# Performance work log

Hardware: AMD Instinct MI355X
Metric: run time of the kernel (lower is better)

## Reference

```python
import jax, jax.numpy as jnp
import numpy as np
from jax import lax

BN_EPS = 1e-3
SLOPE = 0.1
CLUSTER_TEMP = 30.0
K = 16
FEAT = 4096  # 8*8*64


def conv_bn_lrelu(x, w, b, g, beta, m, v):
    # Conv2d stride 2, padding 1 (NCHW / OIHW), then eval-mode BatchNorm, then LeakyReLU.
    y = lax.conv_general_dilated(x, w, window_strides=(2, 2), padding=((1, 1), (1, 1)),
                                 dimension_numbers=("NCHW", "OIHW", "NCHW"))
    y = y + b[None, :, None, None]
    scale = g / jnp.sqrt(v + BN_EPS)
    y = y * scale[None, :, None, None] + (beta - m * scale)[None, :, None, None]
    return jnp.where(y > 0, y, SLOPE * y)


def soft_kmeans(data, mu, num_iter, ct):
    # Row L2-normalize (equivalent to diag(1/||x||) @ data)
    data = data / jnp.linalg.norm(data, axis=1, keepdims=True)
    for _ in range(num_iter):
        dist = data @ mu.T                      # [N, K]
        r = jax.nn.softmax(ct * dist, axis=1)   # [N, K]
        mu = (r.T @ data) / r.sum(axis=0)[:, None]  # [K, F]
    dist = data @ mu.T
    r = jax.nn.softmax(ct * dist, axis=1)
    return mu, r, dist


def setup_inputs() -> dict:
    key = jax.random.key(0)
    ks = jax.random.split(key, 12)
    d = {}
    d["x"] = jax.random.normal(ks[0], (256, 3, 64, 64), dtype=jnp.float32)
    # conv1: 3 -> 128
    d["conv1_w"] = jax.random.normal(ks[1], (128, 3, 3, 3), dtype=jnp.float32) * 0.05
    d["conv1_b"] = jnp.zeros((128,), jnp.float32)
    d["bn1_g"] = jnp.ones((128,), jnp.float32)
    d["bn1_b"] = jnp.zeros((128,), jnp.float32)
    d["bn1_m"] = jax.random.normal(ks[2], (128,), dtype=jnp.float32) * 0.1
    d["bn1_v"] = jax.random.uniform(ks[3], (128,), minval=0.5, maxval=1.5, dtype=jnp.float32)
    # conv2: 128 -> 256
    d["conv2_w"] = jax.random.normal(ks[4], (256, 128, 3, 3), dtype=jnp.float32) * 0.02
    d["conv2_b"] = jnp.zeros((256,), jnp.float32)
    d["bn2_g"] = jnp.ones((256,), jnp.float32)
    d["bn2_b"] = jnp.zeros((256,), jnp.float32)
    d["bn2_m"] = jax.random.normal(ks[5], (256,), dtype=jnp.float32) * 0.1
    d["bn2_v"] = jax.random.uniform(ks[6], (256,), minval=0.5, maxval=1.5, dtype=jnp.float32)
    # conv3: 256 -> 64
    d["conv3_w"] = jax.random.normal(ks[7], (64, 256, 3, 3), dtype=jnp.float32) * 0.02
    d["conv3_b"] = jnp.zeros((64,), jnp.float32)
    d["bn3_g"] = jnp.ones((64,), jnp.float32)
    d["bn3_b"] = jnp.zeros((64,), jnp.float32)
    d["bn3_m"] = jax.random.normal(ks[8], (64,), dtype=jnp.float32) * 0.1
    d["bn3_v"] = jax.random.uniform(ks[9], (64,), minval=0.5, maxval=1.5, dtype=jnp.float32)
    # initial cluster centers, torch.rand(K, F)
    d["mu0"] = jax.random.uniform(ks[10], (K, FEAT), dtype=jnp.float32)
    d["num_iter"] = 10
    return d


def reference(x, conv1_w, conv1_b, bn1_g, bn1_b, bn1_m, bn1_v,
              conv2_w, conv2_b, bn2_g, bn2_b, bn2_m, bn2_v,
              conv3_w, conv3_b, bn3_g, bn3_b, bn3_m, bn3_v,
              mu0, num_iter):
    h = conv_bn_lrelu(x, conv1_w, conv1_b, bn1_g, bn1_b, bn1_m, bn1_v)   # [B,128,32,32]
    h = conv_bn_lrelu(h, conv2_w, conv2_b, bn2_g, bn2_b, bn2_m, bn2_v)   # [B,256,16,16]
    h = conv_bn_lrelu(h, conv3_w, conv3_b, bn3_g, bn3_b, bn3_m, bn3_v)   # [B,64,8,8]
    embeds = h.reshape(-1, FEAT)                                          # [B, 4096]
    mu_init, _, _ = soft_kmeans(embeds, mu0, num_iter, CLUSTER_TEMP)
    _, r, _ = soft_kmeans(embeds, lax.stop_gradient(mu_init), 1, CLUSTER_TEMP)
    return r
```

## Files before the change

kernel.cpp:

```cpp
#include <hip/hip_runtime.h>
#include <stdint.h>
#include <stddef.h>

typedef unsigned short u16;
typedef __attribute__((ext_vector_type(8))) short short8;
typedef __attribute__((ext_vector_type(4))) float f32x4;
typedef __attribute__((ext_vector_type(4))) int int4v;

__device__ __forceinline__ float bf2f(u16 u) {
    unsigned x = ((unsigned)u) << 16;
    return __uint_as_float(x);
}
__device__ __forceinline__ u16 f2bf(float f) {
    unsigned x = __float_as_uint(f);
    unsigned r = (x + 0x7fffu + ((x >> 16) & 1u)) >> 16;
    return (u16)r;
}
__device__ __forceinline__ float ldin(const void* p, size_t i, int isbf) {
    return isbf ? bf2f(((const u16*)p)[i]) : ((const float*)p)[i];
}
__device__ __forceinline__ int detect_bf(const void* v1) {
    const u16* ub = (const u16*)v1;
    int ok = 1;
#pragma unroll
    for (int i = 0; i < 16; i++) {
        float f = bf2f(ub[i]);
        if (!(f >= 0.4f && f <= 1.6f)) ok = 0;
    }
    return ok;
}
__device__ __forceinline__ int sw(int r, int c8) {
    return r * 32 + (((c8) ^ (r & 3)) << 3);
}

struct PrepArgs {
    const void *w1, *w2, *w3;
    u16 *W1p, *W2p, *W3p;
    const void *b1, *g1, *be1, *m1, *v1;
    const void *b2, *g2, *be2, *m2, *v2;
    const void *b3, *g3, *be3, *m3, *v3;
    float *es1, *esh1, *es2, *esh2, *es3, *esh3;
    u16 *zb;
};
__device__ __forceinline__ void packw_body(const void* src, u16* dst, int CI, int Kp,
                                           int total, int blk, int t, int isbf) {
    int p = blk * 256 + t;
    if (p >= total) return;
    int co = p / Kp, k = p - co * Kp;
    int tap = k / CI, ci = k - tap * CI;
    u16 v = 0;
    if (tap < 9) {
        size_t si = (size_t)(co * CI + ci) * 9 + tap;
        v = isbf ? ((const u16*)src)[si] : f2bf(((const float*)src)[si]);
    }
    dst[p] = v;
}
__global__ __launch_bounds__(256) void kprep_all(PrepArgs A) {
    int b = blockIdx.x, t = threadIdx.x;
    int isbf = detect_bf(A.v1);
    if (b < 1152) {
        packw_body(A.w2, A.W2p, 128, 1152, 256 * 1152, b, t, isbf);
    } else if (b < 1728) {
        packw_body(A.w3, A.W3p, 256, 2304, 64 * 2304, b - 1152, t, isbf);
    } else if (b < 1744) {
        packw_body(A.w1, A.W1p, 3, 32, 128 * 32, b - 1728, t, isbf);
    } else {
        if (b == 1745) A.zb[t] = 0;
        int u = (b - 1744) * 256 + t;
        const void *bb, *g, *be, *m, *v;
        float *es, *esh;
        int c;
        if (u < 128)      { c = u;       bb=A.b1; g=A.g1; be=A.be1; m=A.m1; v=A.v1; es=A.es1; esh=A.esh1; }
        else if (u < 384) { c = u - 128; bb=A.b2; g=A.g2; be=A.be2; m=A.m2; v=A.v2; es=A.es2; esh=A.esh2; }
        else if (u < 448) { c = u - 384; bb=A.b3; g=A.g3; be=A.be3; m=A.m3; v=A.v3; es=A.es3; esh=A.esh3; }
        else return;
        float sc = ldin(g, c, isbf) / sqrtf(ldin(v, c, isbf) + 1e-3f);
        float sh = (ldin(bb, c, isbf) - ldin(m, c, isbf)) * sc + ldin(be, c, isbf);
        es[c] = sc;
        esh[c] = sh;
    }
}

__global__ void kfallback(u16* __restrict__ out) {
    int i = blockIdx.x * 256 + threadIdx.x;
    if (i < 4096) out[i] = f2bf(0.0625f);
}

__global__ __launch_bounds__(256) void im2col1(const void* __restrict__ x,
                                               u16* __restrict__ A1,
                                               const void* __restrict__ v1ref) {
    int n = blockIdx.x, t = threadIdx.x;
    int isbf = detect_bf(v1ref);
    __shared__ u16 xs[3 * 64 * 64];
    if (isbf) {
        const u16* xp = (const u16*)x + (size_t)n * 12288;
#pragma unroll
        for (int i = t * 8; i < 12288; i += 2048)
            *(int4v*)&xs[i] = *(const int4v*)&xp[i];
    } else {
        const float* xp = (const float*)x + (size_t)n * 12288;
#pragma unroll
        for (int i = t * 4; i < 12288; i += 1024) {
            float4 v = *(const float4*)&xp[i];
            xs[i] = f2bf(v.x); xs[i + 1] = f2bf(v.y);
            xs[i + 2] = f2bf(v.z); xs[i + 3] = f2bf(v.w);
        }
    }
    __syncthreads();
#pragma unroll
    for (int rr = 0; rr < 4; rr++) {
        int m = rr * 256 + t;
        int ox = m & 31, oy = m >> 5;
        alignas(16) u16 row[32];
#pragma unroll
        for (int k = 0; k < 32; k++) {
            u16 val = 0;
            if (k < 27) {
                int tap = k / 3, ci = k - 3 * tap;
                int ky = tap / 3, kx = tap - 3 * ky;
                int iy = 2 * oy - 1 + ky, ix = 2 * ox - 1 + kx;
                if ((unsigned)iy < 64u && (unsigned)ix < 64u)
                    val = xs[ci * 4096 + iy * 64 + ix];
            }
            row[k] = val;
        }
        int4v* dst = (int4v*)(A1 + ((size_t)n * 1024 + m) * 32);
        const int4v* srcv = (const int4v*)row;
#pragma unroll
        for (int q = 0; q < 4; q++) dst[q] = srcv[q];
    }
}

__global__ __launch_bounds__(256) void gemm_conv1(
    const u16* __restrict__ A1, const u16* __restrict__ W,
    const float* __restrict__ es, const float* __restrict__ esh,
    u16* __restrict__ OutB) {
    alignas(16) __shared__ u16 As[128 * 32];
    alignas(16) __shared__ u16 Bs[128 * 32];
    const int t = threadIdx.x;
    const int m0 = blockIdx.x * 128;
    const int lane = t & 63, w = t >> 6;
    const int wm = w & 1, wn = w >> 1;
    const int rA = t >> 2, c8 = t & 3, koff = c8 * 8;

#pragma unroll
    for (int j = 0; j < 2; j++) {
        int4v va = *(const int4v*)(A1 + (size_t)(m0 + j * 64 + rA) * 32 + koff);
        *(int4v*)&As[sw(j * 64 + rA, c8)] = va;
        int4v vb = *(const int4v*)(W + (size_t)(j * 64 + rA) * 32 + koff);
        *(int4v*)&Bs[sw(j * 64 + rA, c8)] = vb;
    }
    __syncthreads();
    const int qc = lane >> 4, fr = lane & 15;
    short8 af[4], bf[4];
#pragma unroll
    for (int i = 0; i < 4; i++) af[i] = *(const short8*)&As[sw(wm * 64 + i * 16 + fr, qc)];
#pragma unroll
    for (int j = 0; j < 4; j++) bf[j] = *(const short8*)&Bs[sw(wn * 64 + j * 16 + fr, qc)];
    f32x4 acc[4][4];
#pragma unroll
    for (int i = 0; i < 4; i++)
#pragma unroll
        for (int j = 0; j < 4; j++) {
#pragma unroll
            for (int q = 0; q < 4; q++) acc[i][j][q] = 0.f;
            acc[i][j] = __builtin_amdgcn_mfma_f32_16x16x32_bf16(af[i], bf[j], acc[i][j], 0, 0, 0);
        }
    float scv[4], shv[4];
#pragma unroll
    for (int j = 0; j < 4; j++) {
        int c = wn * 64 + j * 16 + fr;
        scv[j] = es[c];
        shv[j] = esh[c];
    }
#pragma unroll
    for (int i = 0; i < 4; i++) {
#pragma unroll
        for (int rg = 0; rg < 4; rg++) {
            int m = m0 + wm * 64 + i * 16 + qc * 4 + rg;
            int ox = m & 31, oy = (m >> 5) & 31, n = m >> 10;
            u16* orow = OutB + ((size_t)(n * 32 + oy) * 32 + ox) * 128 + wn * 64 + fr;
#pragma unroll
            for (int j = 0; j < 4; j++) {
                float v = acc[i][j][rg] * scv[j] + shv[j];
                v = (v > 0.f) ? v : 0.1f * v;
                orow[j * 16] = f2bf(v);
            }
        }
    }
}

__global__ __launch_bounds__(512, 2) void gemm_conv2(
    const u16* __restrict__ h1, const u16* __restrict__ W,
    const float* __restrict__ es, const float* __restrict__ esh,
    u16* __restrict__ OutB, const u16* __restrict__ zb) {
    alignas(16) __shared__ u16 smem[4 * 16384];
    u16* const Ab0 = smem;
    u16* const Ab1 = smem + 16384;
    u16* const Bb0 = smem + 32768;
    u16* const Bb1 = smem + 49152;

    const int t = threadIdx.x;
    const int w = t >> 6, l = t & 63;
    const int img = blockIdx.x;
    const int wm = w >> 2, wn = w & 3;
    const int fr = l & 15, qc = l >> 4;

    int aiy0[4], aix0[4], ac8e[4];
    int brow[4];
#pragma unroll
    for (int i = 0; i < 4; ++i) {
        int gi = w * 256 + i * 64 + l;
        int r = gi >> 3, c8d = gi & 7;
        int c8s = c8d ^ (r & 7);
        int oy = r >> 4, ox = r & 15;
        aiy0[i] = 2 * oy - 1;
        aix0[i] = 2 * ox - 1;
        ac8e[i] = c8s * 8;
        brow[i] = r * 1152 + c8s * 8;
    }
    auto mkA = [&](int i, int ky, int kx) -> const u16* {
        int iy = aiy0[i] + ky, ix = aix0[i] + kx;
        if ((unsigned)iy < 32u && (unsigned)ix < 32u)
            return h1 + (size_t)(((img * 32 + iy) * 32 + ix) * 128 + ac8e[i]);
        return zb;
    };
    auto stage = [&](const u16* src, u16* ldsbase, int i) {
        __builtin_amdgcn_global_load_lds(
            (const __attribute__((address_space(1))) void*)src,
            (__attribute__((address_space(3))) void*)(ldsbase + (w * 4 + i) * 512),
            16, 0, 0);
    };

    f32x4 acc[8][4];
#pragma unroll
    for (int mi = 0; mi < 8; ++mi)
#pragma unroll
        for (int nj = 0; nj < 4; ++nj)
#pragma unroll
            for (int q = 0; q < 4; ++q) acc[mi][nj][q] = 0.0f;

    auto do_tile = [&](const u16* A, const u16* B) {
#pragma unroll
        for (int kk = 0; kk < 2; ++kk) {
            const int c8 = kk * 4 + qc;
            short8 a[8], b[4];
#pragma unroll
            for (int q = 0; q < 8; ++q) {
                int row = wm * 128 + q * 16 + fr;
                a[q] = *(const short8*)(A + row * 64 + ((c8 ^ (row & 7)) << 3));
            }
#pragma unroll
            for (int j = 0; j < 4; ++j) {
                int row = wn * 64 + j * 16 + fr;
                b[j] = *(const short8*)(B + row * 64 + ((c8 ^ (row & 7)) << 3));
            }
            __builtin_amdgcn_s_setprio(1);
#pragma unroll
            for (int q = 0; q < 8; ++q)
#pragma unroll
                for (int j = 0; j < 4; ++j)
                    acc[q][j] = __builtin_amdgcn_mfma_f32_16x16x32_bf16(
                        a[q], b[j], acc[q][j], 0, 0, 0);
            __builtin_amdgcn_s_setprio(0);
        }
    };

    const u16* pcur[4];
#pragma unroll
    for (int i = 0; i < 4; ++i) pcur[i] = mkA(i, 0, 0);
#pragma unroll
    for (int i = 0; i < 4; ++i) {
        stage(pcur[i], Ab0, i);
        stage(W + brow[i], Bb0, i);
    }

    for (int tap = 0; tap < 9; ++tap) {
        __syncthreads();
#pragma unroll
        for (int i = 0; i < 4; ++i) {
            stage(pcur[i] + 64, Ab1, i);
            stage(W + brow[i] + (2 * tap + 1) * 64, Bb1, i);
        }
        do_tile(Ab0, Bb0);
        __syncthreads();
        if (tap < 8) {
            const int tap2 = tap + 1;
            const int ky2 = (tap2 >= 6) ? 2 : (tap2 >= 3) ? 1 : 0;
            const int kx2 = tap2 - 3 * ky2;
#pragma unroll
            for (int i = 0; i < 4; ++i) pcur[i] = mkA(i, ky2, kx2);
#pragma unroll
            for (int i = 0; i < 4; ++i) {
                stage(pcur[i], Ab0, i);
                stage(W + brow[i] + (2 * tap + 2) * 64, Bb0, i);
            }
        }
        do_tile(Ab1, Bb1);
    }

    float scv[4], shv[4];
#pragma unroll
    for (int nj = 0; nj < 4; ++nj) {
        int c = wn * 64 + nj * 16 + fr;
        scv[nj] = es[c];
        shv[nj] = esh[c];
    }
#pragma unroll
    for (int mi = 0; mi < 8; ++mi) {
#pragma unroll
        for (int rg = 0; rg < 4; ++rg) {
            int r = wm * 128 + mi * 16 + qc * 4 + rg;
            u16* orow = OutB + ((size_t)img * 256 + r) * 256 + wn * 64 + fr;
#pragma unroll
            for (int nj = 0; nj < 4; ++nj) {
                float v = acc[mi][nj][rg] * scv[nj] + shv[nj];
                v = (v > 0.f) ? v : 0.1f * v;
                orow[nj * 16] = f2bf(v);
            }
        }
    }
}

__global__ __launch_bounds__(256) void gemm_conv3f(
    const u16* __restrict__ Asrc, const u16* __restrict__ W,
    const float* __restrict__ es3, const float* __restrict__ esh3,
    float* __restrict__ dat, u16* __restrict__ datbf) {
    constexpr int CIN = 256, KTOT = 2304, IH = 16;
    constexpr int CC = 8, SM = 2, SN = 2;

    alignas(16) __shared__ u16 As[64 * 32];
    alignas(16) __shared__ u16 Bs[64 * 32];
    __shared__ float red[4];

    const int t = threadIdx.x;
    const int lid = blockIdx.x;
    const int xcd = lid & 7, slot = lid >> 3;
    const int img = xcd * 32 + slot;
    const int m0 = img * 64;
    const int lane = t & 63, w = t >> 6;
    const int wm = w & 1, wn = w >> 1;
    const int rA = t >> 2, c8 = t & 3, koff = c8 * 8;
    const int fr = lane & 15, qc = lane >> 4;

    f32x4 acc[SM][SN];
#pragma unroll
    for (int i = 0; i < SM; i++)
#pragma unroll
        for (int j = 0; j < SN; j++)
#pragma unroll
            for (int q = 0; q < 4; q++) acc[i][j][q] = 0.0f;

    const int aox = rA & 7, aoy = (rA >> 3) & 7;
    auto mkoffs = [&](int tap) -> int {
        int ky = tap / 3, kx = tap - 3 * ky;
        int iy = 2 * aoy - 1 + ky, ix = 2 * aox - 1 + kx;
        if ((unsigned)iy < (unsigned)IH && (unsigned)ix < (unsigned)IH)
            return ((img * IH + iy) * IH + ix) * CIN;
        return -0x40000000;
    };
    const u16* Wrow = W + (size_t)rA * KTOT + koff;

    int offs_cur = mkoffs(0), offs_nxt;
    const int4v zerov = (int4v){0, 0, 0, 0};
    int4v bufA[2], bufB[2];
#pragma unroll
    for (int pp = 0; pp < 2; pp++) {
        bufA[pp] = (offs_cur >= 0)
                       ? *(const int4v*)(Asrc + offs_cur + pp * 32 + koff)
                       : zerov;
        bufB[pp] = *(const int4v*)(Wrow + pp * 32);
    }

    int flat = 0;
    for (int tap = 0; tap < 9; tap++) {
        offs_nxt = (tap < 8) ? mkoffs(tap + 1) : -0x40000000;
#pragma unroll
        for (int cc = 0; cc < CC; cc++, flat++) {
            const int pb_ = flat & 1;
            *(int4v*)&As[sw(rA, c8)] = bufA[pb_];
            *(int4v*)&Bs[sw(rA, c8)] = bufB[pb_];
            __syncthreads();
            {
                const int cc2 = cc + 2;
                const bool intap = (cc2 < CC);
                const int cci = intap ? cc2 : cc2 - CC;
                int o = intap ? offs_cur : offs_nxt;
                bufA[pb_] = (o >= 0) ? *(const int4v*)(Asrc + o + cci * 32 + koff) : zerov;
                const bool wvalid = intap || (tap < 8);
                const int wk = (intap ? tap : tap + 1) * CIN + cci * 32;
                bufB[pb_] = wvalid ? *(const int4v*)(Wrow + wk) : zerov;
            }
            short8 af[SM], bf[SN];
#pragma unroll
            for (int i = 0; i < SM; i++)
                af[i] = *(const short8*)&As[sw(wm * 32 + i * 16 + fr, qc)];
#pragma unroll
            for (int j = 0; j < SN; j++)
                bf[j] = *(const short8*)&Bs[sw(wn * 32 + j * 16 + fr, qc)];
#pragma unroll
            for (int i = 0; i < SM; i++)
#pragma unroll
                for (int j = 0; j < SN; j++)
                    acc[i][j] = __builtin_amdgcn_mfma_f32_16x16x32_bf16(
                        af[i], bf[j], acc[i][j], 0, 0, 0);
            __syncthreads();
        }
        offs_cur = offs_nxt;
    }

    float vals[SM][SN][4];
    float ssq = 0.f;
#pragma unroll
    for (int j = 0; j < SN; j++) {
        int c = wn * 32 + j * 16 + fr;
        float sc = es3[c], sh = esh3[c];
#pragma unroll
        for (int i = 0; i < SM; i++) {
#pragma unroll
            for (int rg = 0; rg < 4; rg++) {
                float v = acc[i][j][rg] * sc + sh;
                v = (v > 0.f) ? v : 0.1f * v;
                vals[i][j][rg] = v;
                ssq += v * v;
            }
        }
    }
#pragma unroll
    for (int off = 32; off > 0; off >>= 1) ssq += __shfl_xor(ssq, off);
    if (lane == 0) red[w] = ssq;
    __syncthreads();
    float inv = 1.0f / sqrtf(red[0] + red[1] + red[2] + red[3]);
#pragma unroll
    for (int j = 0; j < SN; j++) {
        int c = wn * 32 + j * 16 + fr;
#pragma unroll
        for (int i = 0; i < SM; i++) {
#pragma unroll
            for (int rg = 0; rg < 4; rg++) {
                int row = wm * 32 + i * 16 + qc * 4 + rg;
                size_t idx = (size_t)img * 4096 + c * 64 + row;
                float v = vals[i][j][rg] * inv;
                dat[idx] = v;
                datbf[idx] = f2bf(v);
            }
        }
    }
}

__global__ __launch_bounds__(256) void kgr(const u16* __restrict__ dbf,
                                           const float* __restrict__ dat,
                                           const void* __restrict__ mu0,
                                           u16* __restrict__ Ghi,
                                           u16* __restrict__ Glo,
                                           float* __restrict__ rb0,
                                           const void* __restrict__ v1ref) {
    const int b = blockIdx.x, t = threadIdx.x;
    alignas(16) __shared__ u16 As[64 * 32];
    alignas(16) __shared__ u16 Bs[64 * 32];
    __shared__ float part[16][4];
    __shared__ float ds[16];

    if (b < 16) {
        const int m0 = (b & 3) * 64, n0 = (b >> 2) * 64;
        const int lane = t & 63, w = t >> 6;
        const int wm = w & 1, wn = w >> 1;
        const int rA = t >> 2, c8 = t & 3, koff = c8 * 8;

        f32x4 acc[2][2];
#pragma unroll
        for (int i = 0; i < 2; i++)
#pragma unroll
            for (int j = 0; j < 2; j++)
#pragma unroll
                for (int q = 0; q < 4; q++) acc[i][j][q] = 0.0f;

        int4v pa = *(const int4v*)(dbf + (size_t)(m0 + rA) * 4096 + koff);
        int4v pb = *(const int4v*)(dbf + (size_t)(n0 + rA) * 4096 + koff);
        for (int it = 0; it < 128; it++) {
            *(int4v*)&As[sw(rA, c8)] = pa;
            *(int4v*)&Bs[sw(rA, c8)] = pb;
            __syncthreads();
            if (it + 1 < 128) {
                int k = (it + 1) * 32 + koff;
                pa = *(const int4v*)(dbf + (size_t)(m0 + rA) * 4096 + k);
                pb = *(const int4v*)(dbf + (size_t)(n0 + rA) * 4096 + k);
            }
            const int qc = lane >> 4, fr = lane & 15;
            short8 af[2], bf[2];
#pragma unroll
            for (int i = 0; i < 2; i++) af[i] = *(const short8*)&As[sw(wm * 32 + i * 16 + fr, qc)];
#pragma unroll
            for (int j = 0; j < 2; j++) bf[j] = *(const short8*)&Bs[sw(wn * 32 + j * 16 + fr, qc)];
#pragma unroll
            for (int i = 0; i < 2; i++)
#pragma unroll
                for (int j = 0; j < 2; j++)
                    acc[i][j] = __builtin_amdgcn_mfma_f32_16x16x32_bf16(af[i], bf[j], acc[i][j], 0, 0, 0);
            if (it + 1 < 128) __syncthreads();
        }
#pragma unroll
        for (int j = 0; j < 2; j++) {
            int c = n0 + wn * 32 + j * 16 + (lane & 15);
#pragma unroll
            for (int i = 0; i < 2; i++)
#pragma unroll
                for (int rg = 0; rg < 4; rg++) {
                    int row = m0 + wm * 32 + i * 16 + (lane >> 4) * 4 + rg;
                    float v = acc[i][j][rg];
                    u16 hi = f2bf(v);
                    u16 lo = f2bf(v - bf2f(hi));
                    Ghi[(size_t)row * 256 + c] = hi;
                    Glo[(size_t)row * 256 + c] = lo;
                }
        }
    } else {
        const int n = b - 16;
        const int isbf = detect_bf(v1ref);
        const int lane = t & 63, wv = t >> 6;
        float d[16];
#pragma unroll
        for (int j = 0; j < 16; j++) d[j] = dat[(size_t)n * 4096 + j * 256 + t];
#pragma unroll
        for (int k = 0; k < 16; k++) {
            float a = 0.f;
            if (isbf) {
                const u16* mp = (const u16*)mu0 + (size_t)k * 4096;
#pragma unroll
                for (int j = 0; j < 16; j++) a = fmaf(d[j], bf2f(mp[j * 256 + t]), a);
            } else {
                const float* mp = (const float*)mu0 + (size_t)k * 4096;
#pragma unroll
                for (int j = 0; j < 16; j++) a = fmaf(d[j], mp[j * 256 + t], a);
            }
#pragma unroll
            for (int off = 32; off > 0; off >>= 1) a += __shfl_xor(a, off);
            if (lane == 0) part[k][wv] = a;
        }
        __syncthreads();
        if (t < 16) {
            float dk = part[t][0] + part[t][1] + part[t][2] + part[t][3];
            ds[t] = dk;
            __syncthreads();
            float mx = -1e30f;
#pragma unroll
            for (int j = 0; j < 16; j++) mx = fmaxf(mx, ds[j]);
            float sum = 0.f;
#pragma unroll
            for (int j = 0; j < 16; j++) sum += __expf(30.f * (ds[j] - mx));
            rb0[n * 16 + t] = __expf(30.f * (dk - mx)) / sum;
        }
    }
}

__global__ __launch_bounds__(1024) void kmiter(const u16* __restrict__ Ghi,
                                               const u16* __restrict__ Glo,
                                               const float* __restrict__ rb0,
                                               void* __restrict__ dout,
                                               const void* __restrict__ v1ref) {
    const int t = threadIdx.x;
    const int isbf = detect_bf(v1ref);
    const int lane = t & 63, w = t >> 6;
    const int i0 = w * 16;
    const int col = lane & 15;
    const int q = lane >> 4;

    __shared__ float rf[4096];
    __shared__ u16 rThi[16 * 264];
    __shared__ u16 rTlo[16 * 264];
    __shared__ float part[16][17];
    __shared__ float rs[16];

    for (int idx = t; idx < 4096; idx += 1024) {
        float v = rb0[idx];
        rf[idx] = v;
        u16 hi = f2bf(v);
        rThi[(idx & 15) * 264 + (idx >> 4)] = hi;
        rTlo[(idx & 15) * 264 + (idx >> 4)] = f2bf(v - bf2f(hi));
    }
    __syncthreads();

    const u16* Ahirow = Ghi + (size_t)(i0 + col) * 256 + q * 8;
    const u16* Alorow = Glo + (size_t)(i0 + col) * 256 + q * 8;
    for (int iter = 0; iter < 11; iter++) {
        f32x4 acc = {0.f, 0.f, 0.f, 0.f};
#pragma unroll
        for (int ks = 0; ks < 256; ks += 32) {
            short8 ah = *(const short8*)(Ahirow + ks);
            short8 al = *(const short8*)(Alorow + ks);
            short8 bh = *(const short8*)&rThi[col * 264 + ks + q * 8];
            short8 bl = *(const short8*)&rTlo[col * 264 + ks + q * 8];
            acc = __builtin_amdgcn_mfma_f32_16x16x32_bf16(ah, bh, acc, 0, 0, 0);
            acc = __builtin_amdgcn_mfma_f32_16x16x32_bf16(al, bh, acc, 0, 0, 0);
            acc = __builtin_amdgcn_mfma_f32_16x16x32_bf16(ah, bl, acc, 0, 0, 0);
        }
        if (t < 256) {
            int kk = t & 15, g = t >> 4;
            float psum = 0.f;
#pragma unroll
            for (int nn = 0; nn < 16; nn++) psum += rf[(g * 16 + nn) * 16 + kk];
            part[kk][g] = psum;
        }
        __syncthreads();
        if (t < 16) {
            float ssum = 0.f;
#pragma unroll
            for (int g = 0; g < 16; g++) ssum += part[t][g];
            rs[t] = ssum;
        }
        __syncthreads();
        float rsc = rs[col];
        float rv[4];
#pragma unroll
        for (int rg = 0; rg < 4; rg++) {
            float dk = acc[rg] / rsc;
            float mx = dk;
#pragma unroll
            for (int o = 1; o < 16; o <<= 1) mx = fmaxf(mx, __shfl_xor(mx, o));
            float e = __expf(30.f * (dk - mx));
            float ssum = e;
#pragma unroll
            for (int o = 1; o < 16; o <<= 1) ssum += __shfl_xor(ssum, o);
            rv[rg] = e / ssum;
        }
        if (iter < 10) {
            __syncthreads();
#pragma unroll
            for (int rg = 0; rg < 4; rg++) {
                int row = i0 + q * 4 + rg;
                float v = rv[rg];
                rf[row * 16 + col] = v;
                u16 hi = f2bf(v);
                rThi[col * 264 + row] = hi;
                rTlo[col * 264 + row] = f2bf(v - bf2f(hi));
            }
            __syncthreads();
        } else {
#pragma unroll
            for (int rg = 0; rg < 4; rg++) {
                int row = i0 + q * 4 + rg;
                if (isbf) ((u16*)dout)[row * 16 + col] = f2bf(rv[rg]);
                else ((float*)dout)[row * 16 + col] = rv[rg];
            }
        }
    }
}

extern "C" void kernel_launch(void* const* d_in, const int* in_sizes, int n_in,
                              void* d_out, int out_size, void* d_ws, size_t ws_size,
                              hipStream_t stream) {
    const void* x   = d_in[0];
    const void* w1  = d_in[1];
    const void* b1  = d_in[2];
    const void* g1  = d_in[3];
    const void* be1 = d_in[4];
    const void* m1  = d_in[5];
    const void* v1  = d_in[6];
    const void* w2  = d_in[7];
    const void* b2  = d_in[8];
    const void* g2  = d_in[9];
    const void* be2 = d_in[10];
    const void* m2  = d_in[11];
    const void* v2  = d_in[12];
    const void* w3  = d_in[13];
    const void* b3  = d_in[14];
    const void* g3  = d_in[15];
    const void* be3 = d_in[16];
    const void* m3  = d_in[17];
    const void* v3  = d_in[18];
    const void* mu0 = d_in[19];

    char* p = (char*)d_ws;
    size_t used = 0;
    auto alloc = [&](size_t bytes) -> char* {
        char* q = p;
        size_t rb = (bytes + 255) & ~(size_t)255;
        p += rb;
        used += rb;
        return q;
    };
    float* rb0 = (float*)alloc(4096 * 4);
    u16* Ghi = (u16*)alloc((size_t)65536 * 2);
    u16* Glo = (u16*)alloc((size_t)65536 * 2);
    u16* W1p = (u16*)alloc((size_t)128 * 32 * 2);
    u16* W2p = (u16*)alloc((size_t)256 * 1152 * 2);
    u16* W3p = (u16*)alloc((size_t)64 * 2304 * 2);
    float* es1 = (float*)alloc(128 * 4);
    float* esh1 = (float*)alloc(128 * 4);
    float* es2 = (float*)alloc(256 * 4);
    float* esh2 = (float*)alloc(256 * 4);
    float* es3 = (float*)alloc(64 * 4);
    float* esh3 = (float*)alloc(64 * 4);
    u16* zb = (u16*)alloc(512);
    const size_t R1 = (size_t)256 * 32 * 32 * 128 * 2;
    const size_t R2 = (size_t)256 * 16 * 16 * 256 * 2;
    char* reg1 = alloc(R1);
    char* reg2 = alloc(R2);
    u16* h1 = (u16*)reg1;
    u16* A1 = (u16*)reg2;
    u16* h2 = (u16*)reg2;
    float* dat = (float*)reg1;
    u16* datbf = (u16*)(reg1 + 4194304);

    if (used > ws_size) {
        kfallback<<<16, 256, 0, stream>>>((u16*)d_out);
        return;
    }

    PrepArgs pa = {w1, w2, w3, W1p, W2p, W3p,
                   b1, g1, be1, m1, v1, b2, g2, be2, m2, v2, b3, g3, be3, m3, v3,
                   es1, esh1, es2, esh2, es3, esh3, zb};
    kprep_all<<<1746, 256, 0, stream>>>(pa);
    im2col1<<<256, 256, 0, stream>>>(x, A1, v1);
    gemm_conv1<<<dim3(2048), 256, 0, stream>>>(A1, W1p, es1, esh1, h1);
    gemm_conv2<<<dim3(256), 512, 0, stream>>>(h1, W2p, es2, esh2, h2, zb);
    gemm_conv3f<<<dim3(256), 256, 0, stream>>>(h2, W3p, es3, esh3, dat, datbf);
    kgr<<<dim3(272), 256, 0, stream>>>(datbf, dat, mu0, Ghi, Glo, rb0, v1);
    kmiter<<<1, 1024, 0, stream>>>(Ghi, Glo, rb0, d_out, v1);
}
```

Baseline: 277.6 us.

## Drop LDS staging in Gram GEMM and hoist G fragments into registers in kmiter

The Gram-matrix blocks of kgr now load MFMA fragments straight from global memory instead of staging tiles through shared memory with two barriers per k-step. kmiter keeps its Ghi/Glo fragments in registers across all 11 iterations rather than reloading them from global each time. It also computes the column sums of r with shuffles and a per-wave partial array, which removes the extra barriers and the rf buffer. The costs are more register pressure and global loads that are no longer shared or coalesced through LDS.

```diff
diff --git a/kernel.cpp b/kernel.cpp
--- a/kernel.cpp
+++ b/kernel.cpp
@@ -456,8 +456,6 @@
                                            float* __restrict__ rb0,
                                            const void* __restrict__ v1ref) {
     const int b = blockIdx.x, t = threadIdx.x;
-    alignas(16) __shared__ u16 As[64 * 32];
-    alignas(16) __shared__ u16 Bs[64 * 32];
     __shared__ float part[16][4];
     __shared__ float ds[16];
 
@@ -465,7 +463,7 @@
         const int m0 = (b & 3) * 64, n0 = (b >> 2) * 64;
         const int lane = t & 63, w = t >> 6;
         const int wm = w & 1, wn = w >> 1;
-        const int rA = t >> 2, c8 = t & 3, koff = c8 * 8;
+        const int fr = lane & 15, qc = lane >> 4;
 
         f32x4 acc[2][2];
 #pragma unroll
@@ -475,38 +473,32 @@
 #pragma unroll
                 for (int q = 0; q < 4; q++) acc[i][j][q] = 0.0f;
 
-        int4v pa = *(const int4v*)(dbf + (size_t)(m0 + rA) * 4096 + koff);
-        int4v pb = *(const int4v*)(dbf + (size_t)(n0 + rA) * 4096 + koff);
-        for (int it = 0; it < 128; it++) {
-            *(int4v*)&As[sw(rA, c8)] = pa;
-            *(int4v*)&Bs[sw(rA, c8)] = pb;
-            __syncthreads();
-            if (it + 1 < 128) {
-                int k = (it + 1) * 32 + koff;
-                pa = *(const int4v*)(dbf + (size_t)(m0 + rA) * 4096 + k);
-                pb = *(const int4v*)(dbf + (size_t)(n0 + rA) * 4096 + k);
-            }
-            const int qc = lane >> 4, fr = lane & 15;
-            short8 af[2], bf[2];
-#pragma unroll
-            for (int i = 0; i < 2; i++) af[i] = *(const short8*)&As[sw(wm * 32 + i * 16 + fr, qc)];
-#pragma unroll
-            for (int j = 0; j < 2; j++) bf[j] = *(const short8*)&Bs[sw(wn * 32 + j * 16 + fr, qc)];
+        const u16* a0p = dbf + (size_t)(m0 + wm * 32 + fr) * 4096 + qc * 8;
+        const u16* a1p = a0p + 16 * 4096;
+        const u16* b0p = dbf + (size_t)(n0 + wn * 32 + fr) * 4096 + qc * 8;
+        const u16* b1p = b0p + 16 * 4096;
+        for (int ks = 0; ks < 4096; ks += 128) {
+#pragma unroll
+            for (int u = 0; u < 4; u++) {
+                const int o = ks + u * 32;
+                short8 a0 = *(const short8*)(a0p + o);
+                short8 a1 = *(const short8*)(a1p + o);
+                short8 b0 = *(const short8*)(b0p + o);
+                short8 b1 = *(const short8*)(b1p + o);
+                acc[0][0] = __builtin_amdgcn_mfma_f32_16x16x32_bf16(a0, b0, acc[0][0], 0, 0, 0);
+                acc[0][1] = __builtin_amdgcn_mfma_f32_16x16x32_bf16(a0, b1, acc[0][1], 0, 0, 0);
+                acc[1][0] = __builtin_amdgcn_mfma_f32_16x16x32_bf16(a1, b0, acc[1][0], 0, 0, 0);
+                acc[1][1] = __builtin_amdgcn_mfma_f32_16x16x32_bf16(a1, b1, acc[1][1], 0, 0, 0);
+            }
+        }
+#pragma unroll
+        for (int j = 0; j < 2; j++) {
+            int c = n0 + wn * 32 + j * 16 + fr;
 #pragma unroll
             for (int i = 0; i < 2; i++)
 #pragma unroll
-                for (int j = 0; j < 2; j++)
-                    acc[i][j] = __builtin_amdgcn_mfma_f32_16x16x32_bf16(af[i], bf[j], acc[i][j], 0, 0, 0);
-            if (it + 1 < 128) __syncthreads();
-        }
-#pragma unroll
-        for (int j = 0; j < 2; j++) {
-            int c = n0 + wn * 32 + j * 16 + (lane & 15);
-#pragma unroll
-            for (int i = 0; i < 2; i++)
-#pragma unroll
                 for (int rg = 0; rg < 4; rg++) {
-                    int row = m0 + wm * 32 + i * 16 + (lane >> 4) * 4 + rg;
+                    int row = m0 + wm * 32 + i * 16 + qc * 4 + rg;
                     float v = acc[i][j][rg];
                     u16 hi = f2bf(v);
                     u16 lo = f2bf(v - bf2f(hi));
@@ -565,52 +557,53 @@
     const int col = lane & 15;
     const int q = lane >> 4;
 
-    __shared__ float rf[4096];
     __shared__ u16 rThi[16 * 264];
     __shared__ u16 rTlo[16 * 264];
     __shared__ float part[16][17];
-    __shared__ float rs[16];
-
-    for (int idx = t; idx < 4096; idx += 1024) {
-        float v = rb0[idx];
-        rf[idx] = v;
-        u16 hi = f2bf(v);
-        rThi[(idx & 15) * 264 + (idx >> 4)] = hi;
-        rTlo[(idx & 15) * 264 + (idx >> 4)] = f2bf(v - bf2f(hi));
+
+    short8 gh[8], gl[8];
+    {
+        const u16* Ahirow = Ghi + (size_t)(i0 + col) * 256 + q * 8;
+        const u16* Alorow = Glo + (size_t)(i0 + col) * 256 + q * 8;
+#pragma unroll
+        for (int s = 0; s < 8; s++) {
+            gh[s] = *(const short8*)(Ahirow + s * 32);
+            gl[s] = *(const short8*)(Alorow + s * 32);
+        }
+    }
+
+    {
+        float rv[4];
+#pragma unroll
+        for (int rg = 0; rg < 4; rg++) {
+            int row = i0 + q * 4 + rg;
+            float v = rb0[row * 16 + col];
+            rv[rg] = v;
+            u16 hi = f2bf(v);
+            rThi[col * 264 + row] = hi;
+            rTlo[col * 264 + row] = f2bf(v - bf2f(hi));
+        }
+        float s0 = rv[0] + rv[1] + rv[2] + rv[3];
+        s0 += __shfl_xor(s0, 16);
+        s0 += __shfl_xor(s0, 32);
+        if (lane < 16) part[w][lane] = s0;
     }
     __syncthreads();
-
-    const u16* Ahirow = Ghi + (size_t)(i0 + col) * 256 + q * 8;
-    const u16* Alorow = Glo + (size_t)(i0 + col) * 256 + q * 8;
+    float rsc = 0.f;
+#pragma unroll
+    for (int ww = 0; ww < 16; ww++) rsc += part[ww][col];
+
     for (int iter = 0; iter < 11; iter++) {
         f32x4 acc = {0.f, 0.f, 0.f, 0.f};
 #pragma unroll
-        for (int ks = 0; ks < 256; ks += 32) {
-            short8 ah = *(const short8*)(Ahirow + ks);
-            short8 al = *(const short8*)(Alorow + ks);
-            short8 bh = *(const short8*)&rThi[col * 264 + ks + q * 8];
-            short8 bl = *(const short8*)&rTlo[col * 264 + ks + q * 8];
-            acc = __builtin_amdgcn_mfma_f32_16x16x32_bf16(ah, bh, acc, 0, 0, 0);
-            acc = __builtin_amdgcn_mfma_f32_16x16x32_bf16(al, bh, acc, 0, 0, 0);
-            acc = __builtin_amdgcn_mfma_f32_16x16x32_bf16(ah, bl, acc, 0, 0, 0);
-        }
-        if (t < 256) {
-            int kk = t & 15, g = t >> 4;
-            float psum = 0.f;
-#pragma unroll
-            for (int nn = 0; nn < 16; nn++) psum += rf[(g * 16 + nn) * 16 + kk];
-            part[kk][g] = psum;
-        }
-        __syncthreads();
-        if (t < 16) {
-            float ssum = 0.f;
-#pragma unroll
-            for (int g = 0; g < 16; g++) ssum += part[t][g];
-            rs[t] = ssum;
-        }
-        __syncthreads();
-        float rsc = rs[col];
-        float rv[4];
+        for (int s = 0; s < 8; s++) {
+            short8 bh = *(const short8*)&rThi[col * 264 + s * 32 + q * 8];
+            short8 bl = *(const short8*)&rTlo[col * 264 + s * 32 + q * 8];
+            acc = __builtin_amdgcn_mfma_f32_16x16x32_bf16(gh[s], bh, acc, 0, 0, 0);
+            acc = __builtin_amdgcn_mfma_f32_16x16x32_bf16(gl[s], bh, acc, 0, 0, 0);
+            acc = __builtin_amdgcn_mfma_f32_16x16x32_bf16(gh[s], bl, acc, 0, 0, 0);
+        }
+        float nv[4];
 #pragma unroll
         for (int rg = 0; rg < 4; rg++) {
             float dk = acc[rg] / rsc;
@@ -621,26 +614,31 @@
             float ssum = e;
 #pragma unroll
             for (int o = 1; o < 16; o <<= 1) ssum += __shfl_xor(ssum, o);
-            rv[rg] = e / ssum;
+            nv[rg] = e / ssum;
         }
         if (iter < 10) {
             __syncthreads();
 #pragma unroll
             for (int rg = 0; rg < 4; rg++) {
                 int row = i0 + q * 4 + rg;
-                float v = rv[rg];
-                rf[row * 16 + col] = v;
-                u16 hi = f2bf(v);
+                u16 hi = f2bf(nv[rg]);
                 rThi[col * 264 + row] = hi;
-                rTlo[col * 264 + row] = f2bf(v - bf2f(hi));
-            }
+                rTlo[col * 264 + row] = f2bf(nv[rg] - bf2f(hi));
+            }
+            float s0 = nv[0] + nv[1] + nv[2] + nv[3];
+            s0 += __shfl_xor(s0, 16);
+            s0 += __shfl_xor(s0, 32);
+            if (lane < 16) part[w][lane] = s0;
             __syncthreads();
+            rsc = 0.f;
+#pragma unroll
+            for (int ww = 0; ww < 16; ww++) rsc += part[ww][col];
         } else {
 #pragma unroll
             for (int rg = 0; rg < 4; rg++) {
                 int row = i0 + q * 4 + rg;
-                if (isbf) ((u16*)dout)[row * 16 + col] = f2bf(rv[rg]);
-                else ((float*)dout)[row * 16 + col] = rv[rg];
+                if (isbf) ((u16*)dout)[row * 16 + col] = f2bf(nv[rg]);
+                else ((float*)dout)[row * 16 + col] = nv[rg];
             }
         }
     }
```

After: 293.2 us. 5.6% more time.
